# Optimization experiments

Hardware: AMD Instinct MI355X
Metric: run time of the kernel (lower is better)

## Reference

```python
import jax, jax.numpy as jnp
import numpy as np

HEADS = 8

def setup_inputs() -> dict:
    key = jax.random.key(0)
    ks = jax.random.split(key, 6)
    b, c, w, h = 4, 512, 48, 48
    qc, vc = 512, 512
    s = 1.0 / np.sqrt(c)  # orthogonal-init-like scale for 1x1 conv weights
    return {
        "x": jax.random.normal(ks[0], (b, c, w, h), dtype=jnp.float32),
        "Wq": jax.random.normal(ks[1], (qc, c), dtype=jnp.float32) * s,
        "Wk": jax.random.normal(ks[2], (qc, c), dtype=jnp.float32) * s,
        "Wv": jax.random.normal(ks[3], (vc, c), dtype=jnp.float32) * s,
        "Wsc": jax.random.normal(ks[4], (vc, c), dtype=jnp.float32) * s,
        "gamma": jax.random.normal(ks[5], (1, vc, 1, 1), dtype=jnp.float32),
    }


def reference(x, Wq, Wk, Wv, Wsc, gamma):
    b, c, w, h = x.shape
    n = w * h
    dq = Wq.shape[0] // HEADS
    dv = Wv.shape[0] // HEADS
    # 1x1 convs are channel matmuls
    q = jnp.einsum('bchw,oc->bohw', x, Wq).reshape(b, HEADS, dq, n)
    k = jnp.einsum('bchw,oc->bohw', x, Wk).reshape(b, HEADS, dq, n)
    v = jnp.einsum('bchw,oc->bohw', x, Wv).reshape(b, HEADS, dv, n)
    # attention scores over spatial tokens (no scaling in original)
    attn = jax.nn.softmax(jnp.einsum('bhdn,bhdm->bhnm', q, k), axis=-1)
    out = jnp.einsum('bhnm,bhdm->bnhd', attn, v)  # (b, n, heads, dv)
    out = out.reshape(b, w, h, HEADS * dv).transpose(0, 3, 1, 2)  # head-major channels
    sc = jnp.einsum('bchw,oc->bohw', x, Wsc)
    return gamma * out + sc
```

## Files before the change

### kernel.cpp

```cpp
#include <hip/hip_runtime.h>

#define HEADS 8
static constexpr int BSZ = 4;
static constexpr int CCH = 512;
static constexpr int NSP = 2304;
static constexpr int DH  = 64;

typedef _Float16 f16x8 __attribute__((ext_vector_type(8)));
typedef float f32x4 __attribute__((ext_vector_type(4)));
typedef float f32x16 __attribute__((ext_vector_type(16)));
typedef int i32x4 __attribute__((ext_vector_type(4)));
typedef unsigned short u16;
typedef unsigned int u32;

__device__ __forceinline__ u16 f2h(float f) {
  _Float16 h = (_Float16)f;
  return __builtin_bit_cast(u16, h);
}

__device__ __forceinline__ float fexp2(float x) {
  return __builtin_amdgcn_exp2f(x);
}

__device__ __forceinline__ void gl_lds16(const void* g, void* l) {
  __builtin_amdgcn_global_load_lds(
      (const __attribute__((address_space(1))) u32*)g,
      (__attribute__((address_space(3))) u32*)l, 16, 0, 0);
}

__global__ __launch_bounds__(256) void k_cvt(const float* __restrict__ w0,
    const float* __restrict__ w1, const float* __restrict__ w2,
    const float* __restrict__ w3, u16* __restrict__ Wall,
    const float* __restrict__ x, u16* __restrict__ xT) {
  __shared__ u16 t[64][66];
  int gid = blockIdx.x;
  if (gid < 1024) {
    int wsel = gid >> 8, bx = gid & 255;
    const float* src = wsel == 0 ? w0 : wsel == 1 ? w1 : wsel == 2 ? w2 : w3;
    int i = (bx * 256 + threadIdx.x) * 4;
    float4 v = *(const float4*)(src + i);
    ushort4 o;
    o.x = f2h(v.x); o.y = f2h(v.y); o.z = f2h(v.z); o.w = f2h(v.w);
    *(ushort4*)(Wall + (size_t)wsel * CCH * CCH + i) = o;
  } else {
    int g2 = gid - 1024;
    int b = g2 / 288, rem = g2 % 288;
    int c0 = (rem / 36) * 64, n0 = (rem % 36) * 64;
    int col = threadIdx.x & 63, rb = threadIdx.x >> 6;
#pragma unroll
    for (int rr = 0; rr < 16; rr++) {
      int r = rr * 4 + rb;
      t[r][col] = f2h(x[((size_t)b * CCH + c0 + r) * NSP + n0 + col]);
    }
    __syncthreads();
#pragma unroll
    for (int rr = 0; rr < 16; rr++) {
      int r = rr * 4 + rb;
      xT[((size_t)b * NSP + n0 + r) * CCH + c0 + col] = t[col][r];
    }
  }
}

__global__ __launch_bounds__(256) void k_proj(const u16* __restrict__ Wall,
    const u16* __restrict__ xT, u16* __restrict__ Qo, u16* __restrict__ Ko,
    u16* __restrict__ Vo, float* __restrict__ SCo) {
  __shared__ u16 smem[17408];
  u16* At = smem;
  u16* Bt = smem + 8192;
  int z = blockIdx.z, b = z >> 2, wsel = z & 3;
  int o0 = blockIdx.y * 128, n0 = blockIdx.x * 128;
  int tid = threadIdx.x, lane = tid & 63, wv = tid >> 6;
  int wr = wv >> 1, wc = wv & 1;
  const u16* Asrc = Wall + (size_t)wsel * CCH * CCH + (size_t)o0 * CCH;
  const u16* Bsrc = xT + ((size_t)b * NSP + n0) * CCH;
  f32x4 acc[4][4] = {};
  for (int kc = 0; kc < CCH; kc += 64) {
    __syncthreads();
#pragma unroll
    for (int i = 0; i < 4; i++) {
      int ch = (wv * 4 + i) * 64 + lane;
      int row = ch >> 3, cc = ch & 7;
      gl_lds16(Asrc + (size_t)row * CCH + kc + ((cc ^ (row & 7)) << 3), At + (wv * 4 + i) * 512);
      gl_lds16(Bsrc + (size_t)row * CCH + kc + ((cc ^ (row & 7)) << 3), Bt + (wv * 4 + i) * 512);
    }
    __syncthreads();
#pragma unroll
    for (int ks = 0; ks < 2; ks++) {
      f16x8 af[4], bfr[4];
#pragma unroll
      for (int f = 0; f < 4; f++) {
        int orow = wr * 64 + f * 16 + (lane & 15);
        int nrow = wc * 64 + f * 16 + (lane & 15);
        int k8 = (lane >> 4) + ks * 4;
        af[f]  = *(const f16x8*)(At + orow * 64 + ((k8 ^ (orow & 7)) << 3));
        bfr[f] = *(const f16x8*)(Bt + nrow * 64 + ((k8 ^ (nrow & 7)) << 3));
      }
#pragma unroll
      for (int i = 0; i < 4; i++)
#pragma unroll
        for (int j = 0; j < 4; j++)
          acc[i][j] = __builtin_amdgcn_mfma_f32_16x16x32_f16(af[i], bfr[j], acc[i][j], 0, 0, 0);
    }
  }
  if (wsel >= 2) {
#pragma unroll
    for (int i = 0; i < 4; i++)
#pragma unroll
      for (int j = 0; j < 4; j++)
#pragma unroll
        for (int r = 0; r < 4; r++) {
          int o = o0 + wr * 64 + i * 16 + ((lane >> 4) << 2) + r;
          int n = n0 + wc * 64 + j * 16 + (lane & 15);
          size_t idx = ((size_t)b * CCH + o) * NSP + n;
          if (wsel == 3) SCo[idx] = acc[i][j][r];
          else           Vo[idx]  = f2h(acc[i][j][r]);
        }
  } else {
    __syncthreads();
    u16* stash = smem;
    float qs = (wsel == 0) ? 1.4426950408889634f : 1.0f;
#pragma unroll
    for (int i = 0; i < 4; i++)
#pragma unroll
      for (int j = 0; j < 4; j++)
#pragma unroll
        for (int r = 0; r < 4; r++) {
          int ol = wr * 64 + i * 16 + ((lane >> 4) << 2) + r;
          int nl = wc * 64 + j * 16 + (lane & 15);
          stash[nl * 136 + ol] = f2h(acc[i][j][r] * qs);
        }
    __syncthreads();
    u16* dst = wsel ? Ko : Qo;
    int hl = tid >> 7, nn = tid & 127;
    int h = (o0 >> 6) + hl;
    size_t base = ((size_t)(b * HEADS + h) * NSP + n0 + nn) * DH;
#pragma unroll
    for (int c2 = 0; c2 < 8; c2++)
      *(int4*)(dst + base + c2 * 8) = *(const int4*)(stash + nn * 136 + hl * 64 + c2 * 8);
  }
}

__global__ __launch_bounds__(512) void k_attn(const u16* __restrict__ Qw,
    const u16* __restrict__ Kw, const u16* __restrict__ Vw,
    const float* __restrict__ gamma, float* __restrict__ out) {
  __shared__ u16 smem[17408];
  int bh = blockIdx.x, qt = blockIdx.y;
  int b = bh >> 3, h = bh & 7;
  int tid = threadIdx.x, lane = tid & 63, wv = tid >> 6;
  int l31 = lane & 31, hi = lane >> 5;
  int qh = wv & 3, tp = wv >> 2;
  int gid = tid & 255;
  int q0w = qt * 128 + qh * 32;
  const u16* Ksrc = Kw + (size_t)bh * NSP * DH;
  const u16* Vsrc = Vw + ((size_t)b * CCH + h * DH) * NSP;
  u16* PB = smem + tp * 8192;

  int mk = gid >> 3, pk = gid & 7;
  const u16* kc = Ksrc + (tp * 32 + mk) * DH + ((pk ^ (mk & 7)) << 3);
  int dv = gid >> 2, pv = gid & 3;
  const u16* vc = Vsrc + (size_t)dv * NSP + tp * 32 + ((pv ^ ((dv >> 1) & 3)) << 3);

#define STAGE(c)                                   \
  do {                                             \
    gl_lds16(kc, PB + (c) * 4096 + gid * 8);       \
    gl_lds16(vc, PB + (c) * 4096 + 2048 + gid * 8);\
    kc += 64 * DH;                                 \
    vc += 64;                                      \
  } while (0)

  int kswz = l31 & 7, vswz = (l31 >> 1) & 3;
  int kro = l31 * 64;
  int ko[4], vo[2];
#pragma unroll
  for (int kd = 0; kd < 4; kd++) ko[kd] = ((2 * kd + hi) ^ kswz) << 3;
#pragma unroll
  for (int s = 0; s < 2; s++) vo[s] = ((2 * s + hi) ^ vswz) << 3;
  int vr0 = l31 * 32, vr1 = (32 + l31) * 32;

  f16x8 qf[4];
  const u16* Qbase = Qw + ((size_t)bh * NSP + q0w + l31) * DH + hi * 8;
#pragma unroll
  for (int kd = 0; kd < 4; kd++)
    qf[kd] = *(const f16x8*)(Qbase + kd * 16);

  float mrun = -1e30f, lrun = 0.f;
  f32x16 acc0 = {}, acc1 = {};

#define COMPUTE(c)                                                           \
  do {                                                                       \
    const u16* Kc = PB + (c) * 4096;                                         \
    const u16* Vc = Kc + 2048;                                               \
    f32x16 s0 = {};                                                          \
    __builtin_amdgcn_s_setprio(1);                                           \
    _Pragma("unroll")                                                        \
    for (int kd = 0; kd < 4; kd++) {                                         \
      f16x8 k0 = *(const f16x8*)(Kc + kro + ko[kd]);                         \
      s0 = __builtin_amdgcn_mfma_f32_32x32x16_f16(k0, qf[kd], s0, 0, 0, 0);  \
    }                                                                        \
    __builtin_amdgcn_s_setprio(0);                                           \
    float m0a = fmaxf(fmaxf(s0[0], s0[1]), s0[2]);                           \
    float m0b = fmaxf(fmaxf(s0[3], s0[4]), s0[5]);                           \
    float m0c = fmaxf(fmaxf(s0[6], s0[7]), s0[8]);                           \
    float m0d = fmaxf(fmaxf(s0[9], s0[10]), s0[11]);                         \
    float m0e = fmaxf(fmaxf(s0[12], s0[13]), s0[14]);                        \
    float tm = fmaxf(fmaxf(fmaxf(m0a, m0b), fmaxf(m0c, m0d)),                \
                     fmaxf(m0e, s0[15]));                                    \
    tm = fmaxf(tm, __shfl_xor(tm, 32));                                      \
    if (__any(tm > mrun + 11.5f)) {                                          \
      float mnew = fmaxf(mrun, tm);                                          \
      float scl = fexp2(mrun - mnew);                                        \
      mrun = mnew;                                                           \
      lrun *= scl;                                                           \
      _Pragma("unroll")                                                      \
      for (int r = 0; r < 16; r++) {                                         \
        float sq = __shfl(scl, (r & 3) + 8 * (r >> 2) + 4 * hi);             \
        acc0[r] *= sq;                                                       \
        acc1[r] *= sq;                                                       \
      }                                                                      \
    }                                                                        \
    float ts = 0.f;                                                          \
    u32 P2[4][2];                                                            \
    _Pragma("unroll")                                                        \
    for (int s2 = 0; s2 < 4; s2++)                                           \
      _Pragma("unroll")                                                      \
      for (int c2 = 0; c2 < 2; c2++) {                                       \
        float a = fexp2(s0[4 * s2 + 2 * c2] - mrun);                         \
        float bb = fexp2(s0[4 * s2 + 2 * c2 + 1] - mrun);                    \
        ts += a + bb;                                                        \
        P2[s2][c2] = __builtin_bit_cast(u32, __builtin_amdgcn_cvt_pkrtz(a, bb)); \
      }                                                                      \
    ts += __shfl_xor(ts, 32);                                                \
    lrun += ts;                                                              \
    _Pragma("unroll")                                                        \
    for (int s = 0; s < 2; s++) {                                            \
      int x0 = (int)P2[2 * s][0], y0 = (int)P2[2 * s + 1][0];                \
      int x1 = (int)P2[2 * s][1], y1 = (int)P2[2 * s + 1][1];                \
      asm("v_permlane32_swap_b32 %0, %1" : "+v"(x0), "+v"(y0));              \
      asm("v_permlane32_swap_b32 %0, %1" : "+v"(x1), "+v"(y1));              \
      f16x8 pa = __builtin_bit_cast(f16x8, (i32x4){x0, x1, y0, y1});         \
      __builtin_amdgcn_s_setprio(1);                                         \
      {                                                                      \
        f16x8 vb = *(const f16x8*)(Vc + vr0 + vo[s]);                        \
        acc0 = __builtin_amdgcn_mfma_f32_32x32x16_f16(pa, vb, acc0, 0, 0, 0);\
      }                                                                      \
      {                                                                      \
        f16x8 vb = *(const f16x8*)(Vc + vr1 + vo[s]);                        \
        acc1 = __builtin_amdgcn_mfma_f32_32x32x16_f16(pa, vb, acc1, 0, 0, 0);\
      }                                                                      \
      __builtin_amdgcn_s_setprio(0);                                         \
    }                                                                        \
  } while (0)

  STAGE(0);
  __syncthreads();
  for (int i2 = 0; i2 < 18; i2++) {
    STAGE(1);
    COMPUTE(0);
    __syncthreads();
    if (i2 < 17) STAGE(0);
    COMPUTE(1);
    __syncthreads();
  }

  float* sf = (float*)smem;
  if (tp) {
#pragma unroll
    for (int r = 0; r < 16; r++) {
      sf[qh * 2048 + r * 64 + lane] = acc0[r];
      sf[qh * 2048 + (16 + r) * 64 + lane] = acc1[r];
    }
    if (lane < 32) {
      sf[8192 + qh * 64 + l31] = mrun;
      sf[8192 + qh * 64 + 32 + l31] = lrun;
    }
  }
  __syncthreads();
  if (!tp) {
    float mb = sf[8192 + qh * 64 + l31];
    float lb = sf[8192 + qh * 64 + 32 + l31];
    float M = fmaxf(mrun, mb);
    float fa = fexp2(mrun - M), fb = fexp2(mb - M);
    float linv = 1.0f / (lrun * fa + lb * fb);
    fa *= linv; fb *= linv;
    float faq[16], fbq[16];
#pragma unroll
    for (int r = 0; r < 16; r++) {
      int qloc = (r & 3) + 8 * (r >> 2) + 4 * hi;
      faq[r] = __shfl(fa, qloc);
      fbq[r] = __shfl(fb, qloc);
    }
    size_t outbase = ((size_t)b * CCH + h * DH) * NSP;
#pragma unroll
    for (int dblk = 0; dblk < 2; dblk++) {
      int d = dblk * 32 + l31;
      float g = gamma[h * DH + d];
      float* orow = out + outbase + (size_t)d * NSP + q0w;
#pragma unroll
      for (int s2 = 0; s2 < 4; s2++) {
        int n = 8 * s2 + 4 * hi;
        f32x4 o;
#pragma unroll
        for (int t = 0; t < 4; t++) {
          int r = 4 * s2 + t;
          float oa = dblk ? acc1[r] : acc0[r];
          float ob = sf[qh * 2048 + (dblk * 16 + r) * 64 + lane];
          o[t] = (oa * faq[r] + ob * fbq[r]) * g;
        }
        f32x4 sc = *(const f32x4*)(orow + n);
        *(f32x4*)(orow + n) = o + sc;
      }
    }
  }
#undef STAGE
#undef COMPUTE
}

extern "C" void kernel_launch(void* const* d_in, const int* in_sizes, int n_in,
                              void* d_out, int out_size, void* d_ws, size_t ws_size,
                              hipStream_t stream) {
  const float* x     = (const float*)d_in[0];
  const float* Wq    = (const float*)d_in[1];
  const float* Wk    = (const float*)d_in[2];
  const float* Wv    = (const float*)d_in[3];
  const float* Wsc   = (const float*)d_in[4];
  const float* gamma = (const float*)d_in[5];
  float* out = (float*)d_out;

  u16* xT   = (u16*)d_ws;
  u16* Wall = xT + (size_t)BSZ * NSP * CCH;
  u16* Qw   = Wall + (size_t)4 * CCH * CCH;
  u16* Kw   = Qw + (size_t)BSZ * CCH * NSP;
  u16* Vw   = Kw + (size_t)BSZ * CCH * NSP;

  hipLaunchKernelGGL(k_cvt, dim3(1024 + BSZ * (CCH / 64) * (NSP / 64)), dim3(256), 0, stream,
                     Wq, Wk, Wv, Wsc, Wall, x, xT);
  hipLaunchKernelGGL(k_proj, dim3(NSP / 128, CCH / 128, BSZ * 4), dim3(256), 0, stream,
                     Wall, xT, Qw, Kw, Vw, out);
  hipLaunchKernelGGL(k_attn, dim3(BSZ * HEADS, NSP / 128), dim3(512), 0, stream,
                     Qw, Kw, Vw, gamma, out);
}
```

Before: 138.5 us.

## Double-buffer projection GEMM LDS tiles with 32-wide K stages

Result: slower. 146.3 us (+5.6%).

```diff
diff --git a/kernel.cpp b/kernel.cpp
--- a/kernel.cpp
+++ b/kernel.cpp
@@ -65,43 +65,66 @@
     const u16* __restrict__ xT, u16* __restrict__ Qo, u16* __restrict__ Ko,
     u16* __restrict__ Vo, float* __restrict__ SCo) {
   __shared__ u16 smem[17408];
-  u16* At = smem;
-  u16* Bt = smem + 8192;
   int z = blockIdx.z, b = z >> 2, wsel = z & 3;
   int o0 = blockIdx.y * 128, n0 = blockIdx.x * 128;
   int tid = threadIdx.x, lane = tid & 63, wv = tid >> 6;
   int wr = wv >> 1, wc = wv & 1;
   const u16* Asrc = Wall + (size_t)wsel * CCH * CCH + (size_t)o0 * CCH;
   const u16* Bsrc = xT + ((size_t)b * NSP + n0) * CCH;
+
+  int ch1 = tid, ch2 = 256 + tid;
+  int r1 = ch1 >> 2, r2 = ch2 >> 2;
+  int cc1 = (ch1 & 3) ^ (r1 & 3) ^ (((r1 >> 2) & 1) << 1);
+  int cc2 = (ch2 & 3) ^ (r2 & 3) ^ (((r2 >> 2) & 1) << 1);
+  const u16* a1 = Asrc + (size_t)r1 * CCH + (cc1 << 3);
+  const u16* a2 = Asrc + (size_t)r2 * CCH + (cc2 << 3);
+  const u16* b1 = Bsrc + (size_t)r1 * CCH + (cc1 << 3);
+  const u16* b2 = Bsrc + (size_t)r2 * CCH + (cc2 << 3);
+
+#define PSTAGE(c)                                      \
+  do {                                                 \
+    gl_lds16(a1, smem + (c) * 8192 + ch1 * 8);         \
+    gl_lds16(a2, smem + (c) * 8192 + ch2 * 8);         \
+    gl_lds16(b1, smem + (c) * 8192 + 4096 + ch1 * 8);  \
+    gl_lds16(b2, smem + (c) * 8192 + 4096 + ch2 * 8);  \
+    a1 += 32; a2 += 32; b1 += 32; b2 += 32;            \
+  } while (0)
+
+  int kx = (((lane >> 4) ^ (lane & 3) ^ (((lane >> 2) & 1) << 1)) << 3);
   f32x4 acc[4][4] = {};
-  for (int kc = 0; kc < CCH; kc += 64) {
-    __syncthreads();
-#pragma unroll
-    for (int i = 0; i < 4; i++) {
-      int ch = (wv * 4 + i) * 64 + lane;
-      int row = ch >> 3, cc = ch & 7;
-      gl_lds16(Asrc + (size_t)row * CCH + kc + ((cc ^ (row & 7)) << 3), At + (wv * 4 + i) * 512);
-      gl_lds16(Bsrc + (size_t)row * CCH + kc + ((cc ^ (row & 7)) << 3), Bt + (wv * 4 + i) * 512);
-    }
-    __syncthreads();
-#pragma unroll
-    for (int ks = 0; ks < 2; ks++) {
-      f16x8 af[4], bfr[4];
-#pragma unroll
-      for (int f = 0; f < 4; f++) {
-        int orow = wr * 64 + f * 16 + (lane & 15);
-        int nrow = wc * 64 + f * 16 + (lane & 15);
-        int k8 = (lane >> 4) + ks * 4;
-        af[f]  = *(const f16x8*)(At + orow * 64 + ((k8 ^ (orow & 7)) << 3));
-        bfr[f] = *(const f16x8*)(Bt + nrow * 64 + ((k8 ^ (nrow & 7)) << 3));
-      }
-#pragma unroll
-      for (int i = 0; i < 4; i++)
-#pragma unroll
-        for (int j = 0; j < 4; j++)
-          acc[i][j] = __builtin_amdgcn_mfma_f32_16x16x32_f16(af[i], bfr[j], acc[i][j], 0, 0, 0);
-    }
-  }
+
+#define PCOMPUTE(c)                                                          \
+  do {                                                                       \
+    const u16* Ab = smem + (c) * 8192;                                       \
+    const u16* Bb = Ab + 4096;                                               \
+    f16x8 af[4], bfr[4];                                                     \
+    _Pragma("unroll")                                                        \
+    for (int f = 0; f < 4; f++) {                                            \
+      int orow = wr * 64 + f * 16 + (lane & 15);                             \
+      int nrow = wc * 64 + f * 16 + (lane & 15);                             \
+      af[f]  = *(const f16x8*)(Ab + orow * 32 + kx);                         \
+      bfr[f] = *(const f16x8*)(Bb + nrow * 32 + kx);                         \
+    }                                                                        \
+    _Pragma("unroll")                                                        \
+    for (int i = 0; i < 4; i++)                                              \
+      _Pragma("unroll")                                                      \
+      for (int j = 0; j < 4; j++)                                            \
+        acc[i][j] = __builtin_amdgcn_mfma_f32_16x16x32_f16(af[i], bfr[j],    \
+                                                           acc[i][j], 0, 0, 0); \
+  } while (0)
+
+  PSTAGE(0);
+  __syncthreads();
+#pragma unroll 1
+  for (int it = 0; it < 8; it++) {
+    PSTAGE(1);
+    PCOMPUTE(0);
+    __syncthreads();
+    if (it < 7) PSTAGE(0);
+    PCOMPUTE(1);
+    __syncthreads();
+  }
+
   if (wsel >= 2) {
 #pragma unroll
     for (int i = 0; i < 4; i++)
@@ -116,7 +139,6 @@
           else           Vo[idx]  = f2h(acc[i][j][r]);
         }
   } else {
-    __syncthreads();
     u16* stash = smem;
     float qs = (wsel == 0) ? 1.4426950408889634f : 1.0f;
 #pragma unroll
@@ -138,6 +160,8 @@
     for (int c2 = 0; c2 < 8; c2++)
       *(int4*)(dst + base + c2 * 8) = *(const int4*)(stash + nn * 136 + hl * 64 + c2 * 8);
   }
+#undef PSTAGE
+#undef PCOMPUTE
 }
 
 __global__ __launch_bounds__(512) void k_attn(const u16* __restrict__ Qw,
```
